# Kernel tuning notes

Hardware: AMD Instinct MI355X
Metric: run time of the kernel (lower is better)

The kernel has to match this reference:

```python
import jax, jax.numpy as jnp
import numpy as np

NODES = 1024   # LSTM hidden size (nodes)
LAYERS = 5     # LSTM layers
SEQ = 2048     # sequence length
B = 1          # batch (hardcoded by init_hidden in the torch module)
IN_DIM = 30    # 12 + 12 + 6 concatenated features
OUT_DIM = 12   # n_input_state_real
SLOPE = 0.01   # F.leaky_relu default negative slope


def setup_inputs() -> dict:
    key = jax.random.key(0)
    ks = jax.random.split(key, 8)
    s = 0.02
    return dict(
        sim=jax.random.normal(ks[0], (B, SEQ, 12), dtype=jnp.float32),
        real=jax.random.normal(ks[1], (B, SEQ, 12), dtype=jnp.float32),
        act=jax.random.normal(ks[2], (B, SEQ, 6), dtype=jnp.float32),
        W1=jax.random.normal(ks[3], (NODES, IN_DIM), dtype=jnp.float32) * s,
        b1=jnp.zeros((NODES,), dtype=jnp.float32),
        # all LSTM layers have input size NODES (nn.LSTM(nodes, nodes, layers))
        W_ih=jax.random.normal(ks[4], (LAYERS, 4 * NODES, NODES), dtype=jnp.float32) * s,
        W_hh=jax.random.normal(ks[5], (LAYERS, 4 * NODES, NODES), dtype=jnp.float32) * s,
        b_ih=jnp.zeros((LAYERS, 4 * NODES), dtype=jnp.float32),
        b_hh=jnp.zeros((LAYERS, 4 * NODES), dtype=jnp.float32),
        W2=jax.random.normal(ks[6], (OUT_DIM, NODES), dtype=jnp.float32) * s,
        b2=jnp.zeros((OUT_DIM,), dtype=jnp.float32),
        h0=jnp.zeros((LAYERS, B, NODES), dtype=jnp.float32),
        c0=jnp.zeros((LAYERS, B, NODES), dtype=jnp.float32),
    )


def _lstm_layer(x, h0, c0, W_ih, W_hh, b_ih, b_hh):
    # x: [T, B, N]. Precompute input projection for all timesteps (big GEMM),
    # then scan the recurrence. PyTorch gate order: i, f, g, o.
    x_proj = jnp.einsum('tbn,gn->tbg', x, W_ih) + b_ih  # [T, B, 4N]

    def step(carry, xp):
        h, c = carry
        gates = xp + h @ W_hh.T + b_hh
        i, f, g, o = jnp.split(gates, 4, axis=-1)
        c = jax.nn.sigmoid(f) * c + jax.nn.sigmoid(i) * jnp.tanh(g)
        h = jax.nn.sigmoid(o) * jnp.tanh(c)
        return (h, c), h

    _, ys = jax.lax.scan(step, (h0, c0), x_proj)
    return ys  # [T, B, N]


def reference(sim, real, act, W1, b1, W_ih, W_hh, b_ih, b_hh, W2, b2, h0, c0):
    x = jnp.concatenate((sim, real, act), axis=2)      # [B, T, 30]
    x = jax.nn.leaky_relu(x @ W1.T + b1, SLOPE)        # [B, T, N]
    x = x.transpose(1, 0, 2)                           # [T, B, N] (time-major)
    for l in range(LAYERS):
        x = _lstm_layer(x, h0[l], c0[l], W_ih[l], W_hh[l], b_ih[l], b_hh[l])
    x = jax.nn.leaky_relu(x.transpose(1, 0, 2), SLOPE)  # [B, T, N]
    return x @ W2.T + b2                                # [B, T, 12]
```

## Files before the change

kernel.cpp:

```cpp
#include <hip/hip_runtime.h>

#define NODES 1024
#define LAYERS 5
#define SEQ 2048
#define IN_DIM 30
#define OUT_DIM 12
#define SLOPE 0.01f
#define RING_D 16

typedef unsigned long long u64;

__device__ __forceinline__ float sigmoidf_(float x) { return 1.0f / (1.0f + expf(-x)); }

__global__ __launch_bounds__(256) void fc1_kernel(
    const float* __restrict__ sim, const float* __restrict__ realv,
    const float* __restrict__ act, const float* __restrict__ W1,
    const float* __restrict__ b1, float* __restrict__ x_out)
{
    int t = blockIdx.x;
    __shared__ float in_s[IN_DIM];
    int tid = threadIdx.x;
    if (tid < 12) in_s[tid] = sim[t * 12 + tid];
    else if (tid < 24) in_s[tid] = realv[t * 12 + (tid - 12)];
    else if (tid < 30) in_s[tid] = act[t * 6 + (tid - 24)];
    __syncthreads();
    for (int n = tid; n < NODES; n += 256) {
        float acc = b1[n];
        const float* w = W1 + n * IN_DIM;
        #pragma unroll
        for (int k = 0; k < IN_DIM; ++k) acc += w[k] * in_s[k];
        x_out[t * NODES + n] = acc > 0.f ? acc : SLOPE * acc;
    }
}

#define BM 64
#define BN 64
#define BK 16

__global__ __launch_bounds__(256) void xproj_kernel(
    const float* __restrict__ X, const float* __restrict__ W,
    const float* __restrict__ bih, const float* __restrict__ bhh,
    float* __restrict__ XP)
{
    const int GN = 4 * NODES;
    int bm = blockIdx.y;
    int bn = blockIdx.x;
    __shared__ float As[BK][BM];
    __shared__ float Bs[BK][BN];
    int tid = threadIdx.x;
    int tx = tid % 16, ty = tid / 16;
    int arow = tid / 4;
    int acol4 = (tid % 4) * 4;
    float acc[4][4] = {};

    for (int k0 = 0; k0 < NODES; k0 += BK) {
        float4 a = *(const float4*)&X[(size_t)(bm * BM + arow) * NODES + k0 + acol4];
        As[acol4 + 0][arow] = a.x; As[acol4 + 1][arow] = a.y;
        As[acol4 + 2][arow] = a.z; As[acol4 + 3][arow] = a.w;
        float4 b = *(const float4*)&W[(size_t)(bn * BN + arow) * NODES + k0 + acol4];
        Bs[acol4 + 0][arow] = b.x; Bs[acol4 + 1][arow] = b.y;
        Bs[acol4 + 2][arow] = b.z; Bs[acol4 + 3][arow] = b.w;
        __syncthreads();
        #pragma unroll
        for (int k = 0; k < BK; ++k) {
            float ra[4], rb[4];
            #pragma unroll
            for (int m = 0; m < 4; ++m) ra[m] = As[k][ty * 4 + m];
            #pragma unroll
            for (int n = 0; n < 4; ++n) rb[n] = Bs[k][tx * 4 + n];
            #pragma unroll
            for (int m = 0; m < 4; ++m)
                #pragma unroll
                for (int n = 0; n < 4; ++n)
                    acc[m][n] += ra[m] * rb[n];
        }
        __syncthreads();
    }
    #pragma unroll
    for (int m = 0; m < 4; ++m) {
        int t = bm * BM + ty * 4 + m;
        int g0 = bn * BN + tx * 4;
        float4 o;
        o.x = acc[m][0] + bih[g0 + 0] + bhh[g0 + 0];
        o.y = acc[m][1] + bih[g0 + 1] + bhh[g0 + 1];
        o.z = acc[m][2] + bih[g0 + 2] + bhh[g0 + 2];
        o.w = acc[m][3] + bih[g0 + 3] + bhh[g0 + 3];
        *(float4*)&XP[(size_t)t * GN + g0] = o;
    }
}

__global__ __launch_bounds__(512, 2)
void lstm_group_kernel(
    const float* __restrict__ Wih,
    const float* __restrict__ Whh,
    const float* __restrict__ bih,
    const float* __restrict__ bhh,
    const float* __restrict__ XP,
    const float* __restrict__ h0,
    const float* __restrict__ c0,
    float* __restrict__ Yout,
    u64* rings, int l_base, int NL)
{
    __shared__ u64 mir[2][2][16][64];

    const int tid = threadIdx.x;
    const int wave = tid >> 6, lane = tid & 63;
    const int lg = wave >> 2;
    const int q = wave & 3;
    const int j = blockIdx.x * 4 + q;
    const int l = l_base + lg;
    const bool first = (lg == 0);
    const bool last  = (lg == NL - 1);

    float whh[4][16];
    {
        const float* wp = Whh + (size_t)l * 4 * NODES * NODES;
        #pragma unroll
        for (int g = 0; g < 4; ++g)
            #pragma unroll
            for (int k = 0; k < 16; ++k)
                whh[g][k] = wp[(size_t)(g * NODES + j) * NODES + lane + k * 64];
    }
    float wih[4][16];
    if (!first) {
        const float* wp = Wih + (size_t)l * 4 * NODES * NODES;
        #pragma unroll
        for (int g = 0; g < 4; ++g)
            #pragma unroll
            for (int k = 0; k < 16; ++k)
                wih[g][k] = wp[(size_t)(g * NODES + j) * NODES + lane + k * 64];
    }
    float bg[4] = {0.f, 0.f, 0.f, 0.f};
    if (!first) {
        #pragma unroll
        for (int g = 0; g < 4; ++g)
            bg[g] = bih[l * 4 * NODES + g * NODES + j] + bhh[l * 4 * NODES + g * NODES + j];
    }

    for (int idx = tid; idx < 2 * 2 * 16 * 64; idx += blockDim.x)
        ((u64*)mir)[idx] = 0;

    u64* ring_own = rings + (size_t)l * RING_D * NODES;

    float c = c0[l * NODES + j];
    float xpg[4] = {0.f, 0.f, 0.f, 0.f};
    if (first) {
        #pragma unroll
        for (int g = 0; g < 4; ++g) xpg[g] = XP[(size_t)0 * 4 * NODES + g * NODES + j];
    }
    __syncthreads();

    for (int t = 0; t < SEQ; ++t) {
        float gate[4] = {0.f, 0.f, 0.f, 0.f};

        if (t == 0) {
            #pragma unroll
            for (int k = 0; k < 16; ++k) {
                float hh = h0[l * NODES + lane + k * 64];
                #pragma unroll
                for (int g = 0; g < 4; ++g) gate[g] += whh[g][k] * hh;
            }
        } else {
            u64* so = ring_own + (size_t)(t % RING_D) * NODES;
            const int par = t & 1;
            u64 mybuf[4];
            for (;;) {
                #pragma unroll
                for (int kk = 0; kk < 4; ++kk)
                    mybuf[kk] = __hip_atomic_load(&so[lane + (q * 4 + kk) * 64],
                                                  __ATOMIC_RELAXED, __HIP_MEMORY_SCOPE_AGENT);
                bool ok = true;
                #pragma unroll
                for (int kk = 0; kk < 4; ++kk) ok = ok && ((int)(mybuf[kk] >> 32) == t);
                if (ok) break;
            }
            if (!last && t >= 2) {
                const int thresh = t - 2;
                for (;;) {
                    bool ok = true;
                    #pragma unroll
                    for (int qq = 0; qq < 4; ++qq) {
                        u64 v = __hip_atomic_load(&mir[lg + 1][par][qq * 4][lane],
                                                  __ATOMIC_RELAXED, __HIP_MEMORY_SCOPE_WORKGROUP);
                        ok = ok && ((int)(v >> 32) >= thresh);
                    }
                    if (ok) break;
                }
            }
            #pragma unroll
            for (int kk = 0; kk < 4; ++kk)
                __hip_atomic_store(&mir[lg][par][q * 4 + kk][lane], mybuf[kk],
                                   __ATOMIC_RELAXED, __HIP_MEMORY_SCOPE_WORKGROUP);
            u64 vo[16];
            for (;;) {
                bool ok = true;
                #pragma unroll
                for (int k = 0; k < 16; ++k) {
                    vo[k] = __hip_atomic_load(&mir[lg][par][k][lane],
                                              __ATOMIC_RELAXED, __HIP_MEMORY_SCOPE_WORKGROUP);
                    ok = ok && ((int)(vo[k] >> 32) == t);
                }
                if (ok) break;
            }
            #pragma unroll
            for (int k = 0; k < 16; ++k) {
                float hh = __uint_as_float((unsigned)vo[k]);
                #pragma unroll
                for (int g = 0; g < 4; ++g) gate[g] += whh[g][k] * hh;
            }
        }

        if (!first) {
            const int par = (t + 1) & 1;
            u64 vi[16];
            for (;;) {
                bool ok = true;
                #pragma unroll
                for (int k = 0; k < 16; ++k) {
                    vi[k] = __hip_atomic_load(&mir[lg - 1][par][k][lane],
                                              __ATOMIC_RELAXED, __HIP_MEMORY_SCOPE_WORKGROUP);
                    ok = ok && ((int)(vi[k] >> 32) == t + 1);
                }
                if (ok) break;
            }
            #pragma unroll
            for (int k = 0; k < 16; ++k) {
                float xx = __uint_as_float((unsigned)vi[k]);
                #pragma unroll
                for (int g = 0; g < 4; ++g) gate[g] += wih[g][k] * xx;
            }
        }

        #pragma unroll
        for (int g = 0; g < 4; ++g) {
            float acc = gate[g];
            #pragma unroll
            for (int off = 32; off > 0; off >>= 1) acc += __shfl_xor(acc, off);
            gate[g] = acc + (first ? xpg[g] : bg[g]);
        }

        float ig = sigmoidf_(gate[0]);
        float fg = sigmoidf_(gate[1]);
        float gg = tanhf(gate[2]);
        float og = sigmoidf_(gate[3]);
        c = fg * c + ig * gg;
        float h = og * tanhf(c);

        if (lane == 0) {
            u64 pv = ((u64)(unsigned)(t + 1) << 32) | (u64)__float_as_uint(h);
            __hip_atomic_store(&ring_own[(size_t)((t + 1) % RING_D) * NODES + j], pv,
                               __ATOMIC_RELAXED, __HIP_MEMORY_SCOPE_AGENT);
            if (last) Yout[(size_t)t * NODES + j] = h;
        }

        if (first && t + 1 < SEQ) {
            #pragma unroll
            for (int g = 0; g < 4; ++g)
                xpg[g] = XP[(size_t)(t + 1) * 4 * NODES + g * NODES + j];
        }
    }

    if (!last) {
        const int par = SEQ & 1;
        const int thresh = SEQ - 2;
        for (;;) {
            bool ok = true;
            #pragma unroll
            for (int qq = 0; qq < 4; ++qq) {
                u64 v = __hip_atomic_load(&mir[lg + 1][par][qq * 4][lane],
                                          __ATOMIC_RELAXED, __HIP_MEMORY_SCOPE_WORKGROUP);
                ok = ok && ((int)(v >> 32) >= thresh);
            }
            if (ok) break;
        }
        u64* so = ring_own + (size_t)(SEQ % RING_D) * NODES;
        u64 mybuf[4];
        for (;;) {
            #pragma unroll
            for (int kk = 0; kk < 4; ++kk)
                mybuf[kk] = __hip_atomic_load(&so[lane + (q * 4 + kk) * 64],
                                              __ATOMIC_RELAXED, __HIP_MEMORY_SCOPE_AGENT);
            bool ok = true;
            #pragma unroll
            for (int kk = 0; kk < 4; ++kk) ok = ok && ((int)(mybuf[kk] >> 32) == SEQ);
            if (ok) break;
        }
        #pragma unroll
        for (int kk = 0; kk < 4; ++kk)
            __hip_atomic_store(&mir[lg][par][q * 4 + kk][lane], mybuf[kk],
                               __ATOMIC_RELAXED, __HIP_MEMORY_SCOPE_WORKGROUP);
    }
}

__global__ __launch_bounds__(256) void fc2_kernel(
    const float* __restrict__ Y, const float* __restrict__ W2,
    const float* __restrict__ b2, float* __restrict__ out)
{
    int t = blockIdx.x;
    __shared__ float ys[NODES];
    int tid = threadIdx.x;
    for (int n = tid; n < NODES; n += 256) {
        float v = Y[(size_t)t * NODES + n];
        ys[n] = v > 0.f ? v : SLOPE * v;
    }
    __syncthreads();
    int wave = tid >> 6, lane = tid & 63;
    for (int o = wave; o < OUT_DIM; o += 4) {
        float acc = 0.f;
        const float* w = W2 + o * NODES;
        #pragma unroll
        for (int k = 0; k < 16; ++k) acc += w[lane + k * 64] * ys[lane + k * 64];
        #pragma unroll
        for (int off = 32; off > 0; off >>= 1) acc += __shfl_xor(acc, off);
        if (lane == 0) out[t * OUT_DIM + o] = acc + b2[o];
    }
}

extern "C" void kernel_launch(void* const* d_in, const int* in_sizes, int n_in,
                              void* d_out, int out_size, void* d_ws, size_t ws_size,
                              hipStream_t stream) {
    const float* sim  = (const float*)d_in[0];
    const float* relv = (const float*)d_in[1];
    const float* act  = (const float*)d_in[2];
    const float* W1   = (const float*)d_in[3];
    const float* b1   = (const float*)d_in[4];
    const float* W_ih = (const float*)d_in[5];
    const float* W_hh = (const float*)d_in[6];
    const float* b_ih = (const float*)d_in[7];
    const float* b_hh = (const float*)d_in[8];
    const float* W2   = (const float*)d_in[9];
    const float* b2   = (const float*)d_in[10];
    const float* h0   = (const float*)d_in[11];
    const float* c0   = (const float*)d_in[12];
    float* out = (float*)d_out;

    char* ws = (char*)d_ws;
    float* xbuf = (float*)ws;
    float* xp   = (float*)(ws + (size_t)8 * 1024 * 1024);
    float* ya   = (float*)(ws + (size_t)40 * 1024 * 1024);
    u64*   rings = (u64*)(ws + (size_t)48 * 1024 * 1024);

    hipMemsetAsync(rings, 0, (size_t)LAYERS * RING_D * NODES * sizeof(u64), stream);

    fc1_kernel<<<SEQ, 256, 0, stream>>>(sim, relv, act, W1, b1, xbuf);

    xproj_kernel<<<dim3(4 * NODES / BN, SEQ / BM), 256, 0, stream>>>(
        xbuf, W_ih, b_ih, b_hh, xp);
    {
        int l_base = 0, nl = 2;
        void* args[] = { (void*)&W_ih, (void*)&W_hh, (void*)&b_ih, (void*)&b_hh,
                         (void*)&xp, (void*)&h0, (void*)&c0, (void*)&ya,
                         (void*)&rings, (void*)&l_base, (void*)&nl };
        hipLaunchCooperativeKernel((const void*)lstm_group_kernel,
                                   dim3(256), dim3(512), args, 0, stream);
    }

    xproj_kernel<<<dim3(4 * NODES / BN, SEQ / BM), 256, 0, stream>>>(
        ya, W_ih + (size_t)2 * 4 * NODES * NODES,
        b_ih + 2 * 4 * NODES, b_hh + 2 * 4 * NODES, xp);
    {
        int l_base = 2, nl = 2;
        void* args[] = { (void*)&W_ih, (void*)&W_hh, (void*)&b_ih, (void*)&b_hh,
                         (void*)&xp, (void*)&h0, (void*)&c0, (void*)&ya,
                         (void*)&rings, (void*)&l_base, (void*)&nl };
        hipLaunchCooperativeKernel((const void*)lstm_group_kernel,
                                   dim3(256), dim3(512), args, 0, stream);
    }

    xproj_kernel<<<dim3(4 * NODES / BN, SEQ / BM), 256, 0, stream>>>(
        ya, W_ih + (size_t)4 * 4 * NODES * NODES,
        b_ih + 4 * 4 * NODES, b_hh + 4 * 4 * NODES, xp);
    {
        int l_base = 4, nl = 1;
        void* args[] = { (void*)&W_ih, (void*)&W_hh, (void*)&b_ih, (void*)&b_hh,
                         (void*)&xp, (void*)&h0, (void*)&c0, (void*)&xbuf,
                         (void*)&rings, (void*)&l_base, (void*)&nl };
        hipLaunchCooperativeKernel((const void*)lstm_group_kernel,
                                   dim3(256), dim3(256), args, 0, stream);
    }

    fc2_kernel<<<SEQ, 256, 0, stream>>>(xbuf, W2, b2, out);
}
```

Before: 26.33 ms.

## Fuse layers 2-4 into one three-layer wavefront kernel with LDS-resident weights

Runs layers 2, 3 and 4 as a single cooperative wavefront kernel with 768 threads per block (three layer groups), replacing one two-layer and one one-layer launch plus an intermediate xproj GEMM. This removes a full serial pass over the sequence and an extra launch. Register pressure goes up because launch bounds now require 3 waves-per-SIMD occupancy, so the third layer's W_hh slice is moved to LDS (64KB), and the mirror polling is split into halves to reduce live registers. The risk is that LDS reads in the hot loop and possible register spills slow the per-step critical path.

```diff
diff --git a/kernel.cpp b/kernel.cpp
--- a/kernel.cpp
+++ b/kernel.cpp
@@ -89,7 +89,7 @@
     }
 }
 
-__global__ __launch_bounds__(512, 2)
+__global__ __launch_bounds__(768, 3)
 void lstm_group_kernel(
     const float* __restrict__ Wih,
     const float* __restrict__ Whh,
@@ -101,7 +101,8 @@
     float* __restrict__ Yout,
     u64* rings, int l_base, int NL)
 {
-    __shared__ u64 mir[2][2][16][64];
+    __shared__ u64 mir[3][2][16][64];
+    __shared__ float whh_lds[4][4][NODES];
 
     const int tid = threadIdx.x;
     const int wave = tid >> 6, lane = tid & 63;
@@ -111,9 +112,22 @@
     const int l = l_base + lg;
     const bool first = (lg == 0);
     const bool last  = (lg == NL - 1);
+    const bool lds_whh = (NL == 3 && lg == 2);
 
     float whh[4][16];
-    {
+    if (lds_whh) {
+        const float* wp = Whh + (size_t)l * 4 * NODES * NODES;
+        #pragma unroll
+        for (int g = 0; g < 4; ++g) {
+            const float* src = wp + (size_t)(g * NODES + j) * NODES;
+            float* dst = whh_lds[q][g];
+            #pragma unroll
+            for (int v = 0; v < 4; ++v) {
+                int idx = (lane + v * 64) * 4;
+                *(float4*)&dst[idx] = *(const float4*)&src[idx];
+            }
+        }
+    } else {
         const float* wp = Whh + (size_t)l * 4 * NODES * NODES;
         #pragma unroll
         for (int g = 0; g < 4; ++g)
@@ -137,7 +151,7 @@
             bg[g] = bih[l * 4 * NODES + g * NODES + j] + bhh[l * 4 * NODES + g * NODES + j];
     }
 
-    for (int idx = tid; idx < 2 * 2 * 16 * 64; idx += blockDim.x)
+    for (int idx = tid; idx < 3 * 2 * 16 * 64; idx += blockDim.x)
         ((u64*)mir)[idx] = 0;
 
     u64* ring_own = rings + (size_t)l * RING_D * NODES;
@@ -157,8 +171,13 @@
             #pragma unroll
             for (int k = 0; k < 16; ++k) {
                 float hh = h0[l * NODES + lane + k * 64];
-                #pragma unroll
-                for (int g = 0; g < 4; ++g) gate[g] += whh[g][k] * hh;
+                if (lds_whh) {
+                    #pragma unroll
+                    for (int g = 0; g < 4; ++g) gate[g] += whh_lds[q][g][lane + k * 64] * hh;
+                } else {
+                    #pragma unroll
+                    for (int g = 0; g < 4; ++g) gate[g] += whh[g][k] * hh;
+                }
             }
         } else {
             u64* so = ring_own + (size_t)(t % RING_D) * NODES;
@@ -191,43 +210,57 @@
             for (int kk = 0; kk < 4; ++kk)
                 __hip_atomic_store(&mir[lg][par][q * 4 + kk][lane], mybuf[kk],
                                    __ATOMIC_RELAXED, __HIP_MEMORY_SCOPE_WORKGROUP);
-            u64 vo[16];
-            for (;;) {
-                bool ok = true;
+            #pragma unroll
+            for (int half = 0; half < 2; ++half) {
+                u64 vo[8];
+                for (;;) {
+                    bool ok = true;
+                    #pragma unroll
+                    for (int k = 0; k < 8; ++k) {
+                        vo[k] = __hip_atomic_load(&mir[lg][par][half * 8 + k][lane],
+                                                  __ATOMIC_RELAXED, __HIP_MEMORY_SCOPE_WORKGROUP);
+                        ok = ok && ((int)(vo[k] >> 32) == t);
+                    }
+                    if (ok) break;
+                }
                 #pragma unroll
-                for (int k = 0; k < 16; ++k) {
-                    vo[k] = __hip_atomic_load(&mir[lg][par][k][lane],
-                                              __ATOMIC_RELAXED, __HIP_MEMORY_SCOPE_WORKGROUP);
-                    ok = ok && ((int)(vo[k] >> 32) == t);
-                }
-                if (ok) break;
-            }
-            #pragma unroll
-            for (int k = 0; k < 16; ++k) {
-                float hh = __uint_as_float((unsigned)vo[k]);
-                #pragma unroll
-                for (int g = 0; g < 4; ++g) gate[g] += whh[g][k] * hh;
+                for (int k = 0; k < 8; ++k) {
+                    float hh = __uint_as_float((unsigned)vo[k]);
+                    const int kk = half * 8 + k;
+                    if (lds_whh) {
+                        #pragma unroll
+                        for (int g = 0; g < 4; ++g)
+                            gate[g] += whh_lds[q][g][lane + kk * 64] * hh;
+                    } else {
+                        #pragma unroll
+                        for (int g = 0; g < 4; ++g) gate[g] += whh[g][kk] * hh;
+                    }
+                }
             }
         }
 
         if (!first) {
             const int par = (t + 1) & 1;
-            u64 vi[16];
-            for (;;) {
-                bool ok = true;
+            #pragma unroll
+            for (int half = 0; half < 2; ++half) {
+                u64 vi[8];
+                for (;;) {
+                    bool ok = true;
+                    #pragma unroll
+                    for (int k = 0; k < 8; ++k) {
+                        vi[k] = __hip_atomic_load(&mir[lg - 1][par][half * 8 + k][lane],
+                                                  __ATOMIC_RELAXED, __HIP_MEMORY_SCOPE_WORKGROUP);
+                        ok = ok && ((int)(vi[k] >> 32) == t + 1);
+                    }
+                    if (ok) break;
+                }
                 #pragma unroll
-                for (int k = 0; k < 16; ++k) {
-                    vi[k] = __hip_atomic_load(&mir[lg - 1][par][k][lane],
-                                              __ATOMIC_RELAXED, __HIP_MEMORY_SCOPE_WORKGROUP);
-                    ok = ok && ((int)(vi[k] >> 32) == t + 1);
-                }
-                if (ok) break;
-            }
-            #pragma unroll
-            for (int k = 0; k < 16; ++k) {
-                float xx = __uint_as_float((unsigned)vi[k]);
-                #pragma unroll
-                for (int g = 0; g < 4; ++g) gate[g] += wih[g][k] * xx;
+                for (int k = 0; k < 8; ++k) {
+                    float xx = __uint_as_float((unsigned)vi[k]);
+                    const int kk = half * 8 + k;
+                    #pragma unroll
+                    for (int g = 0; g < 4; ++g) gate[g] += wih[g][kk] * xx;
+                }
             }
         }
 
@@ -359,24 +392,12 @@
         ya, W_ih + (size_t)2 * 4 * NODES * NODES,
         b_ih + 2 * 4 * NODES, b_hh + 2 * 4 * NODES, xp);
     {
-        int l_base = 2, nl = 2;
-        void* args[] = { (void*)&W_ih, (void*)&W_hh, (void*)&b_ih, (void*)&b_hh,
-                         (void*)&xp, (void*)&h0, (void*)&c0, (void*)&ya,
-                         (void*)&rings, (void*)&l_base, (void*)&nl };
-        hipLaunchCooperativeKernel((const void*)lstm_group_kernel,
-                                   dim3(256), dim3(512), args, 0, stream);
-    }
-
-    xproj_kernel<<<dim3(4 * NODES / BN, SEQ / BM), 256, 0, stream>>>(
-        ya, W_ih + (size_t)4 * 4 * NODES * NODES,
-        b_ih + 4 * 4 * NODES, b_hh + 4 * 4 * NODES, xp);
-    {
-        int l_base = 4, nl = 1;
+        int l_base = 2, nl = 3;
         void* args[] = { (void*)&W_ih, (void*)&W_hh, (void*)&b_ih, (void*)&b_hh,
                          (void*)&xp, (void*)&h0, (void*)&c0, (void*)&xbuf,
                          (void*)&rings, (void*)&l_base, (void*)&nl };
         hipLaunchCooperativeKernel((const void*)lstm_group_kernel,
-                                   dim3(256), dim3(256), args, 0, stream);
+                                   dim3(256), dim3(768), args, 0, stream);
     }
 
     fc2_kernel<<<SEQ, 256, 0, stream>>>(xbuf, W2, b2, out);
```

Result: slower. 65.66 ms (+149.4%).
